# Kernel optimization log

Measured on AMD Instinct MI355X. Metric: run time of the kernel, lower is better.

## Reference

```python
import jax, jax.numpy as jnp
import numpy as np

B, T, C, HS = 4, 4096, 1024, 64


def setup_inputs() -> dict:
    key = jax.random.key(0)
    kx, kq, kk, kv = jax.random.split(key, 4)
    x = jax.random.normal(kx, (B, T, C), dtype=jnp.float32)
    s = 1.0 / np.sqrt(C)
    Wq = jax.random.normal(kq, (C, HS), dtype=jnp.float32) * s
    Wk = jax.random.normal(kk, (C, HS), dtype=jnp.float32) * s
    Wv = jax.random.normal(kv, (C, HS), dtype=jnp.float32) * s
    return {"x": x, "Wq": Wq, "Wk": Wk, "Wv": Wv}


def reference(x, Wq, Wk, Wv):
    # q,k,v: [B, T, HS]
    q = x @ Wq
    k = x @ Wk
    v = x @ Wv
    scale = k.shape[-1] ** -0.5
    # full T x T causal attention scores, as the torch module materializes
    scores = jnp.einsum('bqh,bkh->bqk', q, k) * scale  # [B, T, T]
    t = x.shape[1]
    causal = jnp.tril(jnp.ones((t, t), dtype=bool))
    scores = jnp.where(causal[None, :, :], scores, -jnp.inf)
    wei = jax.nn.softmax(scores, axis=-1)  # dropout = 0.0 (eval)
    out = jnp.einsum('bqk,bkh->bqh', wei, v)  # [B, T, HS]
    return out
```

## Files before the change

kernel.cpp:

```cpp
#include <hip/hip_runtime.h>
#include <math.h>

#define BB 4
#define TT 4096
#define CC 1024
#define HS 64
#define MM (BB*TT)

typedef __attribute__((ext_vector_type(8))) short short8;
typedef __attribute__((ext_vector_type(4))) short short4v;
typedef __attribute__((ext_vector_type(4))) float f32x4;
typedef __attribute__((ext_vector_type(4))) unsigned short ushort4v;

__device__ __forceinline__ unsigned short f2bf(float f) {
    union { float f; unsigned u; } v; v.f = f;
    return (unsigned short)((v.u + 0x7fffu + ((v.u >> 16) & 1u)) >> 16);
}

__global__ __launch_bounds__(256) void prep_kernel(
    const float* __restrict__ Wq, const float* __restrict__ Wk,
    const float* __restrict__ Wv, unsigned short* __restrict__ Wt)
{
    const int which = blockIdx.x >> 4;
    const int k0 = (blockIdx.x & 15) * 64;
    const float* __restrict__ W = (which == 0) ? Wq : (which == 1) ? Wk : Wv;
    const float scale = (which == 0) ? 0.125f : 1.0f;
    __shared__ unsigned short lds[64][65];
    const int t = threadIdx.x;
    #pragma unroll
    for (int i = 0; i < 16; i++) {
        int idx = t + 256 * i;
        int r = idx >> 6, n = idx & 63;
        lds[r][n] = f2bf(W[(size_t)(k0 + r) * 64 + n] * scale);
    }
    __syncthreads();
    #pragma unroll
    for (int i = 0; i < 16; i++) {
        int idx = t + 256 * i;
        int n = idx >> 6, r = idx & 63;
        Wt[(which << 16) + (n << 10) + k0 + r] = lds[r][n];
    }
}

__global__ __launch_bounds__(256) void qkv_mfma(
    const float* __restrict__ x, const unsigned short* __restrict__ Wt,
    unsigned short* __restrict__ qb, unsigned short* __restrict__ kb,
    unsigned short* __restrict__ vT)
{
    const int rt = blockIdx.x;
    __shared__ unsigned short xs[2][64][72];

    const int t = threadIdx.x;
    const int w = t >> 6;
    const int lane = t & 63;
    const int quad = lane >> 4;
    const int c = lane & 15;

    const unsigned short* wb[3];
    #pragma unroll
    for (int jj = 0; jj < 3; jj++)
        wb[jj] = Wt + (size_t)((w + 4 * jj) * 16 + c) * CC + quad * 8;

    float4 xreg[4];
    #pragma unroll
    for (int i = 0; i < 4; i++) {
        int idx = t + 256 * i;
        xreg[i] = *(const float4*)(x + (size_t)(rt * 64 + (idx >> 4)) * CC + (idx & 15) * 4);
    }
    short8 wf[3][2];
    #pragma unroll
    for (int jj = 0; jj < 3; jj++)
        #pragma unroll
        for (int ks2 = 0; ks2 < 2; ks2++)
            wf[jj][ks2] = *(const short8*)(wb[jj] + ks2 * 32);

    f32x4 acc[4][3];
    #pragma unroll
    for (int mt = 0; mt < 4; mt++)
        #pragma unroll
        for (int jj = 0; jj < 3; jj++) acc[mt][jj] = (f32x4){0.f, 0.f, 0.f, 0.f};

    for (int k0 = 0; k0 < CC; k0 += 64) {
        const int p = (k0 >> 6) & 1;
        #pragma unroll
        for (int i = 0; i < 4; i++) {
            int idx = t + 256 * i;
            int r = idx >> 4, c4 = (idx & 15) * 4;
            ushort4v pk = { f2bf(xreg[i].x), f2bf(xreg[i].y), f2bf(xreg[i].z), f2bf(xreg[i].w) };
            *(ushort4v*)&xs[p][r][c4] = pk;
        }
        if (k0 + 64 < CC) {
            #pragma unroll
            for (int i = 0; i < 4; i++) {
                int idx = t + 256 * i;
                xreg[i] = *(const float4*)(x + (size_t)(rt * 64 + (idx >> 4)) * CC + k0 + 64 + (idx & 15) * 4);
            }
        }
        __syncthreads();
        short8 wn[3][2];
        if (k0 + 64 < CC) {
            #pragma unroll
            for (int jj = 0; jj < 3; jj++)
                #pragma unroll
                for (int ks2 = 0; ks2 < 2; ks2++)
                    wn[jj][ks2] = *(const short8*)(wb[jj] + k0 + 64 + ks2 * 32);
        }
        #pragma unroll
        for (int ks2 = 0; ks2 < 2; ks2++) {
            short8 af[4];
            #pragma unroll
            for (int mt = 0; mt < 4; mt++)
                af[mt] = *(const short8*)&xs[p][16 * mt + c][ks2 * 32 + quad * 8];
            #pragma unroll
            for (int mt = 0; mt < 4; mt++)
                #pragma unroll
                for (int jj = 0; jj < 3; jj++)
                    acc[mt][jj] = __builtin_amdgcn_mfma_f32_16x16x32_bf16(af[mt], wf[jj][ks2], acc[mt][jj], 0, 0, 0);
        }
        if (k0 + 64 < CC) {
            #pragma unroll
            for (int jj = 0; jj < 3; jj++)
                #pragma unroll
                for (int ks2 = 0; ks2 < 2; ks2++)
                    wf[jj][ks2] = wn[jj][ks2];
        }
    }

    __syncthreads();
    unsigned short (*vtb)[72] = xs[0];
    #pragma unroll
    for (int mt = 0; mt < 4; mt++) {
        #pragma unroll
        for (int reg = 0; reg < 4; reg++) {
            int lrow = 16 * mt + quad * 4 + reg;
            size_t grow = (size_t)(rt * 64 + lrow);
            qb[grow * HS + 16 * w + c] = f2bf(acc[mt][0][reg]);
            kb[grow * HS + 16 * w + c] = f2bf(acc[mt][1][reg]);
            vtb[16 * w + c][lrow] = f2bf(acc[mt][2][reg]);
        }
    }
    __syncthreads();
    {
        const int b  = rt >> 6;
        const int t0 = (rt & 63) * 64;
        #pragma unroll
        for (int i = 0; i < 2; i++) {
            int idx = t + 256 * i;
            int d = idx >> 3, c8 = (idx & 7) * 8;
            *(short8*)(vT + ((size_t)b * HS + d) * TT + t0 + c8) = *(const short8*)&vtb[d][c8];
        }
    }
}

__global__ __launch_bounds__(256, 2) void attn_mfma(
    const unsigned short* __restrict__ qb, const unsigned short* __restrict__ kb,
    const unsigned short* __restrict__ vT, float* __restrict__ Opart,
    float* __restrict__ lpart)
{
    const int bid = blockIdx.x;
    const int qt = (TT / 128 - 1) - (bid >> 4);
    const int j  = (bid >> 2) & 3;
    const int b  = bid & 3;

    __shared__ unsigned short ks[64][72];
    __shared__ unsigned short vt[64][72];

    const int t = threadIdx.x;
    const int w = t >> 6;
    const int lane = t & 63;
    const int quad = lane >> 4;
    const int c = lane & 15;
    const int qrow = qt * 128 + 32 * w;

    short8 aq[2][2];
    #pragma unroll
    for (int qt2 = 0; qt2 < 2; qt2++)
        #pragma unroll
        for (int ksd = 0; ksd < 2; ksd++)
            aq[qt2][ksd] = *(const short8*)(qb + (size_t)(b * TT + qrow + 16 * qt2 + c) * HS + ksd * 32 + quad * 8);

    const int lastkt = 2 * qt + 1;
    const int nkt = (lastkt >= j) ? ((lastkt - j) >> 2) + 1 : 0;
    const unsigned short* Kb = kb + (size_t)b * TT * HS;
    const unsigned short* Vb = vT + (size_t)b * HS * TT;

    short8 kreg[2], vreg[2];
    if (nkt > 0) {
        const int kt0 = j * 64;
        #pragma unroll
        for (int i = 0; i < 2; i++) {
            int idx = t + 256 * i;
            int row = idx >> 3, c8 = (idx & 7) * 8;
            kreg[i] = *(const short8*)(Kb + (size_t)(kt0 + row) * HS + c8);
            vreg[i] = *(const short8*)(Vb + (size_t)row * TT + kt0 + c8);
        }
    }

    float lsum[2] = {0.f, 0.f};
    f32x4 oacc[2][4];
    #pragma unroll
    for (int qt2 = 0; qt2 < 2; qt2++)
        #pragma unroll
        for (int dt = 0; dt < 4; dt++) oacc[qt2][dt] = (f32x4){0.f, 0.f, 0.f, 0.f};

    for (int it = 0; it < nkt; it++) {
        const int kt0 = (j + 4 * it) * 64;
        __syncthreads();
        #pragma unroll
        for (int i = 0; i < 2; i++) {
            int idx = t + 256 * i;
            int row = idx >> 3, c8 = (idx & 7) * 8;
            *(short8*)&ks[row][c8] = kreg[i];
            int t32 = c8 & 32, r32 = c8 & 31;
            int p0 = t32 + ((r32 & 8) << 1) + ((r32 >> 4) << 2);
            short8 v = vreg[i];
            short4v lo = { v[0], v[1], v[2], v[3] };
            short4v hi = { v[4], v[5], v[6], v[7] };
            *(short4v*)&vt[row][p0]     = lo;
            *(short4v*)&vt[row][p0 + 8] = hi;
        }
        if (it + 1 < nkt) {
            const int nb = kt0 + 256;
            #pragma unroll
            for (int i = 0; i < 2; i++) {
                int idx = t + 256 * i;
                int row = idx >> 3, c8 = (idx & 7) * 8;
                kreg[i] = *(const short8*)(Kb + (size_t)(nb + row) * HS + c8);
                vreg[i] = *(const short8*)(Vb + (size_t)row * TT + nb + c8);
            }
        }
        __syncthreads();

        if (kt0 <= qrow + 31) {
            f32x4 sc[4][2];
            #pragma unroll
            for (int st = 0; st < 4; st++)
                #pragma unroll
                for (int qt2 = 0; qt2 < 2; qt2++) sc[st][qt2] = (f32x4){0.f, 0.f, 0.f, 0.f};
            #pragma unroll
            for (int ksd = 0; ksd < 2; ksd++) {
                short8 kf[4];
                #pragma unroll
                for (int st = 0; st < 4; st++)
                    kf[st] = *(const short8*)&ks[16 * st + c][ksd * 32 + quad * 8];
                #pragma unroll
                for (int st = 0; st < 4; st++)
                    #pragma unroll
                    for (int qt2 = 0; qt2 < 2; qt2++)
                        sc[st][qt2] = __builtin_amdgcn_mfma_f32_16x16x32_bf16(kf[st], aq[qt2][ksd], sc[st][qt2], 0, 0, 0);
            }
            const bool needmask = (kt0 + 63 > qrow);
            #pragma unroll
            for (int st = 0; st < 4; st++)
                #pragma unroll
                for (int qt2 = 0; qt2 < 2; qt2++)
                    #pragma unroll
                    for (int reg = 0; reg < 4; reg++) {
                        float p;
                        if (needmask) {
                            int key = kt0 + 16 * st + quad * 4 + reg;
                            int qg  = qrow + 16 * qt2 + c;
                            p = (key <= qg) ? __expf(sc[st][qt2][reg]) : 0.f;
                        } else {
                            p = __expf(sc[st][qt2][reg]);
                        }
                        sc[st][qt2][reg] = p;
                        lsum[qt2] += p;
                    }
            short8 pf[2][2];
            #pragma unroll
            for (int qt2 = 0; qt2 < 2; qt2++)
                #pragma unroll
                for (int t32 = 0; t32 < 2; t32++) {
                    short8 pk;
                    #pragma unroll
                    for (int reg = 0; reg < 4; reg++) {
                        pk[reg]     = (short)f2bf(sc[2 * t32][qt2][reg]);
                        pk[reg + 4] = (short)f2bf(sc[2 * t32 + 1][qt2][reg]);
                    }
                    pf[qt2][t32] = pk;
                }
            #pragma unroll
            for (int t32 = 0; t32 < 2; t32++) {
                short8 vf[4];
                #pragma unroll
                for (int dt = 0; dt < 4; dt++)
                    vf[dt] = *(const short8*)&vt[16 * dt + c][t32 * 32 + quad * 8];
                #pragma unroll
                for (int dt = 0; dt < 4; dt++)
                    #pragma unroll
                    for (int qt2 = 0; qt2 < 2; qt2++)
                        oacc[qt2][dt] = __builtin_amdgcn_mfma_f32_16x16x32_bf16(vf[dt], pf[qt2][t32], oacc[qt2][dt], 0, 0, 0);
            }
        }
    }

    #pragma unroll
    for (int qt2 = 0; qt2 < 2; qt2++) {
        lsum[qt2] += __shfl_xor(lsum[qt2], 16);
        lsum[qt2] += __shfl_xor(lsum[qt2], 32);
    }
    float* __restrict__ Oj = Opart + (size_t)(j * 4 + b) * HS * TT;
    #pragma unroll
    for (int qt2 = 0; qt2 < 2; qt2++)
        #pragma unroll
        for (int dt = 0; dt < 4; dt++)
            #pragma unroll
            for (int reg = 0; reg < 4; reg++) {
                int d = 16 * dt + quad * 4 + reg;
                Oj[(size_t)d * TT + qrow + 16 * qt2 + c] = oacc[qt2][dt][reg];
            }
    if (lane < 16)
        #pragma unroll
        for (int qt2 = 0; qt2 < 2; qt2++)
            lpart[(size_t)(j * 4 + b) * TT + qrow + 16 * qt2 + lane] = lsum[qt2];
}

__global__ __launch_bounds__(256) void combine_kernel(
    const float* __restrict__ Opart, const float* __restrict__ lpart,
    float* __restrict__ out)
{
    const int b  = blockIdx.x & 3;
    const int q0 = (blockIdx.x >> 2) * 64;
    __shared__ float ts[64][68];
    const int t = threadIdx.x;

    float4 s[4] = {};
    #pragma unroll
    for (int jj = 0; jj < 4; jj++) {
        const float* Oj = Opart + (size_t)(jj * 4 + b) * HS * TT;
        #pragma unroll
        for (int i = 0; i < 4; i++) {
            int idx = t + 256 * i;
            int d = idx >> 4, c4 = (idx & 15) * 4;
            float4 v = *(const float4*)(Oj + (size_t)d * TT + q0 + c4);
            s[i].x += v.x; s[i].y += v.y; s[i].z += v.z; s[i].w += v.w;
        }
    }
    #pragma unroll
    for (int i = 0; i < 4; i++) {
        int idx = t + 256 * i;
        int d = idx >> 4, c4 = (idx & 15) * 4;
        *(float4*)&ts[d][c4] = s[i];
    }
    __syncthreads();

    const int q  = t >> 2;
    const int dc = (t & 3) * 16;
    float l = 0.f;
    #pragma unroll
    for (int jj = 0; jj < 4; jj++)
        l += lpart[(size_t)(jj * 4 + b) * TT + q0 + q];
    const float inv = 1.f / l;
    #pragma unroll
    for (int g = 0; g < 4; g++) {
        float4 r;
        r.x = ts[dc + g * 4 + 0][q] * inv;
        r.y = ts[dc + g * 4 + 1][q] * inv;
        r.z = ts[dc + g * 4 + 2][q] * inv;
        r.w = ts[dc + g * 4 + 3][q] * inv;
        *(float4*)(out + (size_t)(b * TT + q0 + q) * HS + dc + g * 4) = r;
    }
}

extern "C" void kernel_launch(void* const* d_in, const int* in_sizes, int n_in,
                              void* d_out, int out_size, void* d_ws, size_t ws_size,
                              hipStream_t stream) {
    const float* x  = (const float*)d_in[0];
    const float* Wq = (const float*)d_in[1];
    const float* Wk = (const float*)d_in[2];
    const float* Wv = (const float*)d_in[3];
    float* out = (float*)d_out;

    unsigned short* Wt   = (unsigned short*)d_ws;
    unsigned short* qbuf = Wt + 3 * 64 * 1024;
    unsigned short* kbuf = qbuf + (size_t)MM * HS;
    unsigned short* vTb  = kbuf + (size_t)MM * HS;
    float* Opart = (float*)(vTb + (size_t)MM * HS);
    float* lpart = Opart + 4 * (size_t)MM * HS;

    prep_kernel<<<48, 256, 0, stream>>>(Wq, Wk, Wv, Wt);
    qkv_mfma<<<MM / 64, 256, 0, stream>>>(x, Wt, qbuf, kbuf, vTb);
    attn_mfma<<<BB * (TT / 128) * 4, 256, 0, stream>>>(qbuf, kbuf, vTb, Opart, lpart);
    combine_kernel<<<BB * (TT / 64), 256, 0, stream>>>(Opart, lpart, out);
}
```

Before: 151.9 us.

## Halve row tiles in QKV projection and attention to double block counts

The QKV projection now handles 32 rows per block instead of 64, with each wave owning three output column tiles and a smaller LDS buffer. The attention kernel now handles 64 query rows per block instead of 128, with one 16-row tile per wave and higher launch-bound occupancy. Both changes double the grid size to improve load balance and latency hiding across CUs. In exchange, each K/V tile loaded into LDS is reused by fewer queries, so K/V traffic per unit of work rises.

```diff
diff --git a/kernel.cpp b/kernel.cpp
--- a/kernel.cpp
+++ b/kernel.cpp
@@ -42,13 +42,13 @@
     }
 }
 
-__global__ __launch_bounds__(256) void qkv_mfma(
+__global__ __launch_bounds__(256, 2) void qkv_mfma(
     const float* __restrict__ x, const unsigned short* __restrict__ Wt,
     unsigned short* __restrict__ qb, unsigned short* __restrict__ kb,
     unsigned short* __restrict__ vT)
 {
     const int rt = blockIdx.x;
-    __shared__ unsigned short xs[2][64][72];
+    __shared__ unsigned short xs[2][32][72];
 
     const int t = threadIdx.x;
     const int w = t >> 6;
@@ -59,13 +59,13 @@
     const unsigned short* wb[3];
     #pragma unroll
     for (int jj = 0; jj < 3; jj++)
-        wb[jj] = Wt + (size_t)((w + 4 * jj) * 16 + c) * CC + quad * 8;
-
-    float4 xreg[4];
-    #pragma unroll
-    for (int i = 0; i < 4; i++) {
+        wb[jj] = Wt + (size_t)((3 * w + jj) * 16 + c) * CC + quad * 8;
+
+    float4 xreg[2];
+    #pragma unroll
+    for (int i = 0; i < 2; i++) {
         int idx = t + 256 * i;
-        xreg[i] = *(const float4*)(x + (size_t)(rt * 64 + (idx >> 4)) * CC + (idx & 15) * 4);
+        xreg[i] = *(const float4*)(x + (size_t)(rt * 32 + (idx >> 4)) * CC + (idx & 15) * 4);
     }
     short8 wf[3][2];
     #pragma unroll
@@ -74,16 +74,16 @@
         for (int ks2 = 0; ks2 < 2; ks2++)
             wf[jj][ks2] = *(const short8*)(wb[jj] + ks2 * 32);
 
-    f32x4 acc[4][3];
-    #pragma unroll
-    for (int mt = 0; mt < 4; mt++)
+    f32x4 acc[2][3];
+    #pragma unroll
+    for (int mt = 0; mt < 2; mt++)
         #pragma unroll
         for (int jj = 0; jj < 3; jj++) acc[mt][jj] = (f32x4){0.f, 0.f, 0.f, 0.f};
 
     for (int k0 = 0; k0 < CC; k0 += 64) {
         const int p = (k0 >> 6) & 1;
         #pragma unroll
-        for (int i = 0; i < 4; i++) {
+        for (int i = 0; i < 2; i++) {
             int idx = t + 256 * i;
             int r = idx >> 4, c4 = (idx & 15) * 4;
             ushort4v pk = { f2bf(xreg[i].x), f2bf(xreg[i].y), f2bf(xreg[i].z), f2bf(xreg[i].w) };
@@ -91,9 +91,9 @@
         }
         if (k0 + 64 < CC) {
             #pragma unroll
-            for (int i = 0; i < 4; i++) {
+            for (int i = 0; i < 2; i++) {
                 int idx = t + 256 * i;
-                xreg[i] = *(const float4*)(x + (size_t)(rt * 64 + (idx >> 4)) * CC + k0 + 64 + (idx & 15) * 4);
+                xreg[i] = *(const float4*)(x + (size_t)(rt * 32 + (idx >> 4)) * CC + k0 + 64 + (idx & 15) * 4);
             }
         }
         __syncthreads();
@@ -107,12 +107,12 @@
         }
         #pragma unroll
         for (int ks2 = 0; ks2 < 2; ks2++) {
-            short8 af[4];
-            #pragma unroll
-            for (int mt = 0; mt < 4; mt++)
+            short8 af[2];
+            #pragma unroll
+            for (int mt = 0; mt < 2; mt++)
                 af[mt] = *(const short8*)&xs[p][16 * mt + c][ks2 * 32 + quad * 8];
             #pragma unroll
-            for (int mt = 0; mt < 4; mt++)
+            for (int mt = 0; mt < 2; mt++)
                 #pragma unroll
                 for (int jj = 0; jj < 3; jj++)
                     acc[mt][jj] = __builtin_amdgcn_mfma_f32_16x16x32_bf16(af[mt], wf[jj][ks2], acc[mt][jj], 0, 0, 0);
@@ -127,38 +127,42 @@
     }
 
     __syncthreads();
-    unsigned short (*vtb)[72] = xs[0];
-    #pragma unroll
-    for (int mt = 0; mt < 4; mt++) {
-        #pragma unroll
-        for (int reg = 0; reg < 4; reg++) {
-            int lrow = 16 * mt + quad * 4 + reg;
-            size_t grow = (size_t)(rt * 64 + lrow);
-            qb[grow * HS + 16 * w + c] = f2bf(acc[mt][0][reg]);
-            kb[grow * HS + 16 * w + c] = f2bf(acc[mt][1][reg]);
-            vtb[16 * w + c][lrow] = f2bf(acc[mt][2][reg]);
+    unsigned short (*vtb)[36] = (unsigned short (*)[36])xs;
+    #pragma unroll
+    for (int jj = 0; jj < 3; jj++) {
+        const int n = 3 * w + jj;
+        const int which = n >> 2;
+        const int col0 = (n & 3) * 16;
+        #pragma unroll
+        for (int mt = 0; mt < 2; mt++) {
+            #pragma unroll
+            for (int reg = 0; reg < 4; reg++) {
+                int lrow = 16 * mt + quad * 4 + reg;
+                if (which == 0)
+                    qb[(size_t)(rt * 32 + lrow) * HS + col0 + c] = f2bf(acc[mt][jj][reg]);
+                else if (which == 1)
+                    kb[(size_t)(rt * 32 + lrow) * HS + col0 + c] = f2bf(acc[mt][jj][reg]);
+                else
+                    vtb[col0 + c][lrow] = f2bf(acc[mt][jj][reg]);
+            }
         }
     }
     __syncthreads();
     {
-        const int b  = rt >> 6;
-        const int t0 = (rt & 63) * 64;
-        #pragma unroll
-        for (int i = 0; i < 2; i++) {
-            int idx = t + 256 * i;
-            int d = idx >> 3, c8 = (idx & 7) * 8;
-            *(short8*)(vT + ((size_t)b * HS + d) * TT + t0 + c8) = *(const short8*)&vtb[d][c8];
-        }
-    }
-}
-
-__global__ __launch_bounds__(256, 2) void attn_mfma(
+        const int b  = rt >> 7;
+        const int t0 = (rt & 127) * 32;
+        int d = t >> 2, c8 = (t & 3) * 8;
+        *(short8*)(vT + ((size_t)b * HS + d) * TT + t0 + c8) = *(const short8*)&vtb[d][c8];
+    }
+}
+
+__global__ __launch_bounds__(256, 4) void attn_mfma(
     const unsigned short* __restrict__ qb, const unsigned short* __restrict__ kb,
     const unsigned short* __restrict__ vT, float* __restrict__ Opart,
     float* __restrict__ lpart)
 {
     const int bid = blockIdx.x;
-    const int qt = (TT / 128 - 1) - (bid >> 4);
+    const int qt = (TT / 64 - 1) - (bid >> 4);
     const int j  = (bid >> 2) & 3;
     const int b  = bid & 3;
 
@@ -170,17 +174,14 @@
     const int lane = t & 63;
     const int quad = lane >> 4;
     const int c = lane & 15;
-    const int qrow = qt * 128 + 32 * w;
-
-    short8 aq[2][2];
-    #pragma unroll
-    for (int qt2 = 0; qt2 < 2; qt2++)
-        #pragma unroll
-        for (int ksd = 0; ksd < 2; ksd++)
-            aq[qt2][ksd] = *(const short8*)(qb + (size_t)(b * TT + qrow + 16 * qt2 + c) * HS + ksd * 32 + quad * 8);
-
-    const int lastkt = 2 * qt + 1;
-    const int nkt = (lastkt >= j) ? ((lastkt - j) >> 2) + 1 : 0;
+    const int qrow = qt * 64 + 16 * w;
+
+    short8 aq[2];
+    #pragma unroll
+    for (int ksd = 0; ksd < 2; ksd++)
+        aq[ksd] = *(const short8*)(qb + (size_t)(b * TT + qrow + c) * HS + ksd * 32 + quad * 8);
+
+    const int nkt = (qt >= j) ? ((qt - j) >> 2) + 1 : 0;
     const unsigned short* Kb = kb + (size_t)b * TT * HS;
     const unsigned short* Vb = vT + (size_t)b * HS * TT;
 
@@ -196,12 +197,10 @@
         }
     }
 
-    float lsum[2] = {0.f, 0.f};
-    f32x4 oacc[2][4];
-    #pragma unroll
-    for (int qt2 = 0; qt2 < 2; qt2++)
-        #pragma unroll
-        for (int dt = 0; dt < 4; dt++) oacc[qt2][dt] = (f32x4){0.f, 0.f, 0.f, 0.f};
+    float lsum = 0.f;
+    f32x4 oacc[4];
+    #pragma unroll
+    for (int dt = 0; dt < 4; dt++) oacc[dt] = (f32x4){0.f, 0.f, 0.f, 0.f};
 
     for (int it = 0; it < nkt; it++) {
         const int kt0 = (j + 4 * it) * 64;
@@ -231,12 +230,10 @@
         }
         __syncthreads();
 
-        if (kt0 <= qrow + 31) {
-            f32x4 sc[4][2];
-            #pragma unroll
-            for (int st = 0; st < 4; st++)
-                #pragma unroll
-                for (int qt2 = 0; qt2 < 2; qt2++) sc[st][qt2] = (f32x4){0.f, 0.f, 0.f, 0.f};
+        if (kt0 <= qrow + 15) {
+            f32x4 sc[4];
+            #pragma unroll
+            for (int st = 0; st < 4; st++) sc[st] = (f32x4){0.f, 0.f, 0.f, 0.f};
             #pragma unroll
             for (int ksd = 0; ksd < 2; ksd++) {
                 short8 kf[4];
@@ -245,41 +242,35 @@
                     kf[st] = *(const short8*)&ks[16 * st + c][ksd * 32 + quad * 8];
                 #pragma unroll
                 for (int st = 0; st < 4; st++)
-                    #pragma unroll
-                    for (int qt2 = 0; qt2 < 2; qt2++)
-                        sc[st][qt2] = __builtin_amdgcn_mfma_f32_16x16x32_bf16(kf[st], aq[qt2][ksd], sc[st][qt2], 0, 0, 0);
+                    sc[st] = __builtin_amdgcn_mfma_f32_16x16x32_bf16(kf[st], aq[ksd], sc[st], 0, 0, 0);
             }
             const bool needmask = (kt0 + 63 > qrow);
             #pragma unroll
             for (int st = 0; st < 4; st++)
                 #pragma unroll
-                for (int qt2 = 0; qt2 < 2; qt2++)
-                    #pragma unroll
-                    for (int reg = 0; reg < 4; reg++) {
-                        float p;
-                        if (needmask) {
-                            int key = kt0 + 16 * st + quad * 4 + reg;
-                            int qg  = qrow + 16 * qt2 + c;
-                            p = (key <= qg) ? __expf(sc[st][qt2][reg]) : 0.f;
-                        } else {
-                            p = __expf(sc[st][qt2][reg]);
-                        }
-                        sc[st][qt2][reg] = p;
-                        lsum[qt2] += p;
+                for (int reg = 0; reg < 4; reg++) {
+                    float p;
+                    if (needmask) {
+                        int key = kt0 + 16 * st + quad * 4 + reg;
+                        int qg  = qrow + c;
+                        p = (key <= qg) ? __expf(sc[st][reg]) : 0.f;
+                    } else {
+                        p = __expf(sc[st][reg]);
                     }
-            short8 pf[2][2];
-            #pragma unroll
-            for (int qt2 = 0; qt2 < 2; qt2++)
-                #pragma unroll
-                for (int t32 = 0; t32 < 2; t32++) {
-                    short8 pk;
-                    #pragma unroll
-                    for (int reg = 0; reg < 4; reg++) {
-                        pk[reg]     = (short)f2bf(sc[2 * t32][qt2][reg]);
-                        pk[reg + 4] = (short)f2bf(sc[2 * t32 + 1][qt2][reg]);
-                    }
-                    pf[qt2][t32] = pk;
+                    sc[st][reg] = p;
+                    lsum += p;
                 }
+            short8 pf[2];
+            #pragma unroll
+            for (int t32 = 0; t32 < 2; t32++) {
+                short8 pk;
+                #pragma unroll
+                for (int reg = 0; reg < 4; reg++) {
+                    pk[reg]     = (short)f2bf(sc[2 * t32][reg]);
+                    pk[reg + 4] = (short)f2bf(sc[2 * t32 + 1][reg]);
+                }
+                pf[t32] = pk;
+            }
             #pragma unroll
             for (int t32 = 0; t32 < 2; t32++) {
                 short8 vf[4];
@@ -288,32 +279,24 @@
                     vf[dt] = *(const short8*)&vt[16 * dt + c][t32 * 32 + quad * 8];
                 #pragma unroll
                 for (int dt = 0; dt < 4; dt++)
-                    #pragma unroll
-                    for (int qt2 = 0; qt2 < 2; qt2++)
-                        oacc[qt2][dt] = __builtin_amdgcn_mfma_f32_16x16x32_bf16(vf[dt], pf[qt2][t32], oacc[qt2][dt], 0, 0, 0);
-            }
-        }
-    }
-
-    #pragma unroll
-    for (int qt2 = 0; qt2 < 2; qt2++) {
-        lsum[qt2] += __shfl_xor(lsum[qt2], 16);
-        lsum[qt2] += __shfl_xor(lsum[qt2], 32);
-    }
+                    oacc[dt] = __builtin_amdgcn_mfma_f32_16x16x32_bf16(vf[dt], pf[t32], oacc[dt], 0, 0, 0);
+            }
+        }
+    }
+
+    lsum += __shfl_xor(lsum, 16);
+    lsum += __shfl_xor(lsum, 32);
+
     float* __restrict__ Oj = Opart + (size_t)(j * 4 + b) * HS * TT;
     #pragma unroll
-    for (int qt2 = 0; qt2 < 2; qt2++)
-        #pragma unroll
-        for (int dt = 0; dt < 4; dt++)
-            #pragma unroll
-            for (int reg = 0; reg < 4; reg++) {
-                int d = 16 * dt + quad * 4 + reg;
-                Oj[(size_t)d * TT + qrow + 16 * qt2 + c] = oacc[qt2][dt][reg];
-            }
+    for (int dt = 0; dt < 4; dt++)
+        #pragma unroll
+        for (int reg = 0; reg < 4; reg++) {
+            int d = 16 * dt + quad * 4 + reg;
+            Oj[(size_t)d * TT + qrow + c] = oacc[dt][reg];
+        }
     if (lane < 16)
-        #pragma unroll
-        for (int qt2 = 0; qt2 < 2; qt2++)
-            lpart[(size_t)(j * 4 + b) * TT + qrow + 16 * qt2 + lane] = lsum[qt2];
+        lpart[(size_t)(j * 4 + b) * TT + qrow + lane] = lsum;
 }
 
 __global__ __launch_bounds__(256) void combine_kernel(
@@ -380,7 +363,7 @@
     float* lpart = Opart + 4 * (size_t)MM * HS;
 
     prep_kernel<<<48, 256, 0, stream>>>(Wq, Wk, Wv, Wt);
-    qkv_mfma<<<MM / 64, 256, 0, stream>>>(x, Wt, qbuf, kbuf, vTb);
-    attn_mfma<<<BB * (TT / 128) * 4, 256, 0, stream>>>(qbuf, kbuf, vTb, Opart, lpart);
+    qkv_mfma<<<MM / 32, 256, 0, stream>>>(x, Wt, qbuf, kbuf, vTb);
+    attn_mfma<<<BB * (TT / 64) * 4, 256, 0, stream>>>(qbuf, kbuf, vTb, Opart, lpart);
     combine_kernel<<<BB * (TT / 64), 256, 0, stream>>>(Opart, lpart, out);
 }
```

Result: faster. 147.4 us (-2.9%).
